# Performance work log

Measured on AMD Instinct MI355X. Metric: run time of the kernel, lower is better.

The kernel has to match this reference:

```python
import jax, jax.numpy as jnp
import numpy as np

B, DIM, IMG, HEADS, DH = 8, 512, 32, 8, 64
INNER = HEADS * DH  # == DIM, required by final reshape(b, n, c)
N = IMG * IMG
BN_EPS = 1e-5


def setup_inputs() -> dict:
    key = jax.random.key(0)
    ks = jax.random.split(key, 11)
    s = lambda k, sh: jax.random.normal(k, sh, jnp.float32) * 0.05
    return {
        "x": jax.random.normal(ks[0], (B, N, DIM), jnp.float32),
        # stacked q/k/v params, index 0=q, 1=k, 2=v
        "dw_w": s(ks[1], (3, DIM, 1, 3, 3)),   # depthwise conv kernels (OIHW, groups=DIM)
        "dw_b": s(ks[2], (3, DIM)),
        "bn_g": jnp.ones((3, DIM), jnp.float32) + s(ks[3], (3, DIM)),
        "bn_b": s(ks[4], (3, DIM)),
        "bn_m": s(ks[5], (3, DIM)),
        "bn_v": jnp.abs(jax.random.normal(ks[6], (3, DIM), jnp.float32)) + 1.0,
        "pw_w": s(ks[7], (3, INNER, DIM)),     # pointwise 1x1 conv weights
        "pw_b": s(ks[8], (3, INNER)),
        "out_w": s(ks[9], (DIM, INNER)),       # nn.Linear weight [out, in]
        "out_b": s(ks[10], (DIM,)),
    }


def _proj(x_img, dw_w, dw_b, bn_g, bn_b, bn_m, bn_v, pw_w, pw_b):
    # depthwise 3x3 conv, stride 1, pad 1
    y = jax.lax.conv_general_dilated(
        x_img, dw_w, (1, 1), [(1, 1), (1, 1)],
        dimension_numbers=("NCHW", "OIHW", "NCHW"), feature_group_count=DIM)
    y = y + dw_b[None, :, None, None]
    # eval-mode BatchNorm2d
    scale = bn_g / jnp.sqrt(bn_v + BN_EPS)
    y = (y - bn_m[None, :, None, None]) * scale[None, :, None, None] + bn_b[None, :, None, None]
    # pointwise 1x1 conv
    y = jnp.einsum("bchw,oc->bohw", y, pw_w) + pw_b[None, :, None, None]
    return y


def reference(x, dw_w, dw_b, bn_g, bn_b, bn_m, bn_v, pw_w, pw_b, out_w, out_b):
    b = x.shape[0]
    # b (l w) c -> b c l w
    xi = x.transpose(0, 2, 1).reshape(b, DIM, IMG, IMG)
    # q, k, v: b (h d) l w -> b h (l w) d
    qkv = [
        _proj(xi, dw_w[i], dw_b[i], bn_g[i], bn_b[i], bn_m[i], bn_v[i], pw_w[i], pw_b[i])
        .reshape(b, HEADS, DH, N).transpose(0, 1, 3, 2)
        for i in range(3)
    ]
    q, k, v = qkv
    att = jax.nn.softmax(jnp.einsum("bhnd,bhmd->bhnm", q, k) * (DH ** -0.5), axis=-1)
    out = jnp.einsum("bhnm,bhmd->bhnd", att, v)  # [b,h,n,d]
    out = out.transpose(0, 2, 1, 3).reshape(b, N, INNER)
    return out @ out_w.T + out_b  # to_out Linear (dropout=0)
```

## Files before the change

### kernel.cpp

```cpp
#include <hip/hip_runtime.h>
#include <hip/hip_bf16.h>

#define BB    8
#define DIMC  512
#define IMGS  32
#define NPIX  1024
#define NHEAD 8
#define DHEAD 64

typedef __attribute__((ext_vector_type(8))) short short8;
typedef __attribute__((ext_vector_type(4))) float float4v;

__device__ __forceinline__ float b2f(unsigned short u) {
  union { unsigned int i; float f; } c;
  c.i = ((unsigned int)u) << 16;
  return c.f;
}
__device__ __forceinline__ unsigned short f2b(float f) {
  union { float f; unsigned int u; } c;
  c.f = f;
  unsigned int r = c.u + 0x7fffu + ((c.u >> 16) & 1u);
  return (unsigned short)(r >> 16);
}

__device__ __forceinline__ void storeC(float* p, float v) { *p = v; }
__device__ __forceinline__ void storeC(unsigned short* p, float v) { *p = f2b(v); }

__device__ __forceinline__ void async16(const void* g, void* l) {
  __builtin_amdgcn_global_load_lds(
      (const __attribute__((address_space(1))) void*)g,
      (__attribute__((address_space(3))) void*)l, 16, 0, 0);
}

__global__ __launch_bounds__(256) void wcvt_kernel(
    const float* __restrict__ pw_w, const float* __restrict__ out_w,
    unsigned short* __restrict__ wbf) {
  const int i4 = (blockIdx.x * 256 + threadIdx.x) * 4;
  float4 v = (i4 < 3 * DIMC * DIMC)
                 ? *reinterpret_cast<const float4*>(pw_w + i4)
                 : *reinterpret_cast<const float4*>(out_w + (i4 - 3 * DIMC * DIMC));
  ushort4 o;
  o.x = f2b(v.x); o.y = f2b(v.y); o.z = f2b(v.z); o.w = f2b(v.w);
  *reinterpret_cast<ushort4*>(wbf + i4) = o;
}

__global__ __launch_bounds__(256) void dwbn_kernel(
    const float* __restrict__ x, const float* __restrict__ dw_w,
    const float* __restrict__ dw_b, const float* __restrict__ bn_g,
    const float* __restrict__ bn_b, const float* __restrict__ bn_m,
    const float* __restrict__ bn_v, unsigned short* __restrict__ z) {
  const int bx = blockIdx.x;
  const int b = bx >> 10, n = bx & (NPIX - 1);
  const int l = n >> 5, w = n & 31;
  const int c0 = threadIdx.x * 2;
  const float* xb = x + (size_t)b * NPIX * DIMC + c0;
  float2 xv[9];
  #pragma unroll
  for (int kh = 0; kh < 3; ++kh) {
    #pragma unroll
    for (int kw = 0; kw < 3; ++kw) {
      const int l2 = l + kh - 1, w2 = w + kw - 1;
      const bool ok = (l2 >= 0 && l2 < IMGS && w2 >= 0 && w2 < IMGS);
      xv[kh * 3 + kw] =
          ok ? *reinterpret_cast<const float2*>(xb + (size_t)(l2 * IMGS + w2) * DIMC)
             : make_float2(0.f, 0.f);
    }
  }
  #pragma unroll
  for (int i = 0; i < 3; ++i) {
    const int pc = i * DIMC + c0;
    const float* wp = dw_w + (size_t)pc * 9;
    float a0 = dw_b[pc], a1 = dw_b[pc + 1];
    #pragma unroll
    for (int k = 0; k < 9; ++k) {
      a0 = fmaf(wp[k], xv[k].x, a0);
      a1 = fmaf(wp[9 + k], xv[k].y, a1);
    }
    const float s0 = bn_g[pc] * rsqrtf(bn_v[pc] + 1e-5f);
    const float s1 = bn_g[pc + 1] * rsqrtf(bn_v[pc + 1] + 1e-5f);
    const float r0 = (a0 - bn_m[pc]) * s0 + bn_b[pc];
    const float r1 = (a1 - bn_m[pc + 1]) * s1 + bn_b[pc + 1];
    ushort2 st;
    st.x = f2b(r0);
    st.y = f2b(r1);
    *reinterpret_cast<ushort2*>(
        z + (((size_t)(i * BB + b)) * NPIX + n) * DIMC + c0) = st;
  }
}

template <typename CT>
__global__ __launch_bounds__(256) void gemm_mfma(
    const unsigned short* __restrict__ Abase,
    const unsigned short* __restrict__ Wbase,
    const float* __restrict__ biasBase, CT* __restrict__ Cbase) {
  __shared__ short As[8 * 64 * 8];
  __shared__ short Bs[8 * 64 * 8];
  const int bz = blockIdx.z;
  const int wi = bz >> 3;
  const short* A = (const short*)Abase + (size_t)bz * NPIX * DIMC;
  const short* W = (const short*)Wbase + (size_t)wi * DIMC * DIMC;
  const float* bias = biasBase + wi * DIMC;
  CT* C = Cbase + (size_t)bz * NPIX * DIMC;

  const int t = threadIdx.x;
  const int wv = t >> 6, lane = t & 63;
  const int lo = lane & 15, hi = lane >> 4;
  const int wm = wv >> 1, wn = wv & 1;
  const int m0 = blockIdx.y * 128, n0 = blockIdx.x * 128;

  float4v acc[4][4];
  #pragma unroll
  for (int i = 0; i < 4; ++i)
    #pragma unroll
    for (int j = 0; j < 4; ++j) acc[i][j] = {0.f, 0.f, 0.f, 0.f};

  for (int k0 = 0; k0 < DIMC; k0 += 32) {
    #pragma unroll
    for (int p = 0; p < 2; ++p) {
      const int sub = wv + p * 4;
      async16(A + (size_t)(m0 + sub * 16 + lo) * DIMC + k0 + hi * 8,
              As + (sub * 64 + lane) * 8);
      async16(W + (size_t)(n0 + sub * 16 + lo) * DIMC + k0 + hi * 8,
              Bs + (sub * 64 + lane) * 8);
    }
    __syncthreads();
    short8 af[4], bf[4];
    #pragma unroll
    for (int mt = 0; mt < 4; ++mt)
      af[mt] = *reinterpret_cast<const short8*>(As + ((wm * 4 + mt) * 64 + lane) * 8);
    #pragma unroll
    for (int nt = 0; nt < 4; ++nt)
      bf[nt] = *reinterpret_cast<const short8*>(Bs + ((wn * 4 + nt) * 64 + lane) * 8);
    #pragma unroll
    for (int mt = 0; mt < 4; ++mt)
      #pragma unroll
      for (int nt = 0; nt < 4; ++nt)
        acc[mt][nt] = __builtin_amdgcn_mfma_f32_16x16x32_bf16(af[mt], bf[nt],
                                                              acc[mt][nt], 0, 0, 0);
    __syncthreads();
  }

  float bv[4];
  #pragma unroll
  for (int nt = 0; nt < 4; ++nt) bv[nt] = bias[n0 + wn * 64 + nt * 16 + lo];
  #pragma unroll
  for (int mt = 0; mt < 4; ++mt) {
    #pragma unroll
    for (int r = 0; r < 4; ++r) {
      const int row = m0 + wm * 64 + mt * 16 + hi * 4 + r;
      CT* cp = C + (size_t)row * DIMC + n0 + wn * 64 + lo;
      #pragma unroll
      for (int nt = 0; nt < 4; ++nt) storeC(cp + nt * 16, acc[mt][nt][r] + bv[nt]);
    }
  }
}

__global__ __launch_bounds__(256) void vt_kernel(
    const unsigned short* __restrict__ v, unsigned short* __restrict__ vt) {
  __shared__ unsigned short tile[64][68];
  const int n0 = blockIdx.x * 64, h = blockIdx.y, b = blockIdx.z;
  const int t = threadIdx.x;
  const unsigned short* vb = v + (size_t)b * NPIX * DIMC + h * DHEAD;
  #pragma unroll
  for (int u = 0; u < 4; ++u) {
    const int lin = t + u * 256;
    const int row = lin >> 4, c4 = (lin & 15) * 4;
    *reinterpret_cast<ushort4*>(&tile[row][c4]) =
        *reinterpret_cast<const ushort4*>(vb + (size_t)(n0 + row) * DIMC + c4);
  }
  __syncthreads();
  unsigned short* vtb = vt + ((size_t)(b * NHEAD + h)) * DHEAD * NPIX;
  #pragma unroll
  for (int u = 0; u < 4; ++u) {
    const int lin = t + u * 256;
    const int d = lin >> 4, n4 = (lin & 15) * 4;
    ushort4 o;
    o.x = tile[n4 + 0][d];
    o.y = tile[n4 + 1][d];
    o.z = tile[n4 + 2][d];
    o.w = tile[n4 + 3][d];
    *reinterpret_cast<ushort4*>(vtb + (size_t)d * NPIX + n0 + n4) = o;
  }
}

__global__ __launch_bounds__(256) void attn_mfma(
    const unsigned short* __restrict__ qkv, const unsigned short* __restrict__ vt,
    unsigned short* __restrict__ attn_o) {
  __shared__ short Ks[8 * 64 * 8];
  __shared__ short VTs[8 * 64 * 8];
  __shared__ short Ps[4 * 16 * 72];

  const int qt = blockIdx.x, h = blockIdx.y, b = blockIdx.z;
  const int t = threadIdx.x;
  const int wv = t >> 6, lane = t & 63;
  const int lo = lane & 15, hi = lane >> 4;
  short* Ps_w = Ps + wv * 16 * 72;

  const short* qb = (const short*)qkv + ((size_t)(0 * BB + b) * NPIX) * DIMC + h * DHEAD;
  const short* kb = (const short*)qkv + ((size_t)(1 * BB + b) * NPIX) * DIMC + h * DHEAD;
  const short* vtb = (const short*)vt + ((size_t)(b * NHEAD + h)) * DHEAD * NPIX;

  short8 qfrag[2];
  #pragma unroll
  for (int cc = 0; cc < 2; ++cc)
    qfrag[cc] = *reinterpret_cast<const short8*>(
        qb + (size_t)(qt * 64 + wv * 16 + lo) * DIMC + cc * 32 + hi * 8);

  float m_prev[4], l_run[4];
  float4v oacc[4];
  #pragma unroll
  for (int r = 0; r < 4; ++r) { m_prev[r] = -3.0e38f; l_run[r] = 0.f; }
  #pragma unroll
  for (int dt = 0; dt < 4; ++dt) oacc[dt] = {0.f, 0.f, 0.f, 0.f};

  for (int kt = 0; kt < 16; ++kt) {
    #pragma unroll
    for (int p = 0; p < 2; ++p) {
      const int sub = wv + p * 4;
      const int nk = sub >> 1, cc = sub & 1;
      async16(kb + (size_t)(kt * 64 + nk * 16 + lo) * DIMC + cc * 32 + hi * 8,
              Ks + (sub * 64 + lane) * 8);
      async16(vtb + (size_t)(nk * 16 + lo) * NPIX + kt * 64 + cc * 32 + hi * 8,
              VTs + (sub * 64 + lane) * 8);
    }
    __syncthreads();

    float4v sacc[4];
    #pragma unroll
    for (int nt = 0; nt < 4; ++nt) {
      sacc[nt] = {0.f, 0.f, 0.f, 0.f};
      const short8 k0 = *reinterpret_cast<const short8*>(Ks + ((nt * 2 + 0) * 64 + lane) * 8);
      const short8 k1 = *reinterpret_cast<const short8*>(Ks + ((nt * 2 + 1) * 64 + lane) * 8);
      sacc[nt] = __builtin_amdgcn_mfma_f32_16x16x32_bf16(qfrag[0], k0, sacc[nt], 0, 0, 0);
      sacc[nt] = __builtin_amdgcn_mfma_f32_16x16x32_bf16(qfrag[1], k1, sacc[nt], 0, 0, 0);
    }

    float alpha[4];
    #pragma unroll
    for (int r = 0; r < 4; ++r) {
      const float s0 = sacc[0][r] * 0.125f, s1 = sacc[1][r] * 0.125f;
      const float s2 = sacc[2][r] * 0.125f, s3 = sacc[3][r] * 0.125f;
      float ml = fmaxf(fmaxf(s0, s1), fmaxf(s2, s3));
      ml = fmaxf(ml, __shfl_xor(ml, 1));
      ml = fmaxf(ml, __shfl_xor(ml, 2));
      ml = fmaxf(ml, __shfl_xor(ml, 4));
      ml = fmaxf(ml, __shfl_xor(ml, 8));
      const float mn = fmaxf(m_prev[r], ml);
      const float al = __expf(m_prev[r] - mn);
      const float p0 = __expf(s0 - mn), p1 = __expf(s1 - mn);
      const float p2 = __expf(s2 - mn), p3 = __expf(s3 - mn);
      short* pr = Ps_w + (hi * 4 + r) * 72 + lo;
      pr[0]  = (short)f2b(p0);
      pr[16] = (short)f2b(p1);
      pr[32] = (short)f2b(p2);
      pr[48] = (short)f2b(p3);
      float ps = p0 + p1 + p2 + p3;
      ps += __shfl_xor(ps, 1);
      ps += __shfl_xor(ps, 2);
      ps += __shfl_xor(ps, 4);
      ps += __shfl_xor(ps, 8);
      l_run[r] = l_run[r] * al + ps;
      m_prev[r] = mn;
      alpha[r] = al;
    }
    #pragma unroll
    for (int dt = 0; dt < 4; ++dt)
      #pragma unroll
      for (int r = 0; r < 4; ++r) oacc[dt][r] *= alpha[r];
    __syncthreads();

    const short8 pf0 = *reinterpret_cast<const short8*>(Ps_w + lo * 72 + 0 + hi * 8);
    const short8 pf1 = *reinterpret_cast<const short8*>(Ps_w + lo * 72 + 32 + hi * 8);
    #pragma unroll
    for (int dt = 0; dt < 4; ++dt) {
      const short8 v0 = *reinterpret_cast<const short8*>(VTs + ((dt * 2 + 0) * 64 + lane) * 8);
      const short8 v1 = *reinterpret_cast<const short8*>(VTs + ((dt * 2 + 1) * 64 + lane) * 8);
      oacc[dt] = __builtin_amdgcn_mfma_f32_16x16x32_bf16(pf0, v0, oacc[dt], 0, 0, 0);
      oacc[dt] = __builtin_amdgcn_mfma_f32_16x16x32_bf16(pf1, v1, oacc[dt], 0, 0, 0);
    }
    __syncthreads();
  }

  float inv[4];
  #pragma unroll
  for (int r = 0; r < 4; ++r) inv[r] = 1.0f / l_run[r];
  #pragma unroll
  for (int dt = 0; dt < 4; ++dt) {
    #pragma unroll
    for (int r = 0; r < 4; ++r) {
      const int row = qt * 64 + wv * 16 + hi * 4 + r;
      attn_o[((size_t)b * NPIX + row) * DIMC + h * DHEAD + dt * 16 + lo] =
          f2b(oacc[dt][r] * inv[r]);
    }
  }
}

extern "C" void kernel_launch(void* const* d_in, const int* in_sizes, int n_in,
                              void* d_out, int out_size, void* d_ws, size_t ws_size,
                              hipStream_t stream) {
  const float* x    = (const float*)d_in[0];
  const float* dw_w = (const float*)d_in[1];
  const float* dw_b = (const float*)d_in[2];
  const float* bn_g = (const float*)d_in[3];
  const float* bn_b = (const float*)d_in[4];
  const float* bn_m = (const float*)d_in[5];
  const float* bn_v = (const float*)d_in[6];
  const float* pw_w = (const float*)d_in[7];
  const float* pw_b = (const float*)d_in[8];
  const float* out_w = (const float*)d_in[9];
  const float* out_b = (const float*)d_in[10];
  float* out = (float*)d_out;

  unsigned short* z    = (unsigned short*)d_ws;
  unsigned short* qkv  = z + (size_t)3 * BB * NPIX * DIMC;
  unsigned short* wbf  = qkv + (size_t)3 * BB * NPIX * DIMC;
  unsigned short* vtb  = z;
  unsigned short* attn_o = z + (size_t)BB * NHEAD * DHEAD * NPIX;

  wcvt_kernel<<<dim3(1024), 256, 0, stream>>>(pw_w, out_w, wbf);
  dwbn_kernel<<<dim3(BB * NPIX), 256, 0, stream>>>(x, dw_w, dw_b, bn_g, bn_b,
                                                   bn_m, bn_v, z);
  gemm_mfma<unsigned short><<<dim3(4, 8, 24), 256, 0, stream>>>(z, wbf, pw_b, qkv);
  vt_kernel<<<dim3(16, NHEAD, BB), 256, 0, stream>>>(
      qkv + (size_t)2 * BB * NPIX * DIMC, vtb);
  attn_mfma<<<dim3(16, NHEAD, BB), 256, 0, stream>>>(qkv, vtb, attn_o);
  gemm_mfma<float><<<dim3(4, 8, 8), 256, 0, stream>>>(
      attn_o, wbf + (size_t)3 * DIMC * DIMC, out_b, out);
}
```

Measured before the change: 245.1 us.

## Split attention keys across waves, drop online max, fold softmax scale into Q

The attention kernel is restructured so each wave owns a quarter of the keys for all 64 query rows, with private LDS staging. This removes the block-wide barriers inside the key loop, and the partial outputs and row sums are reduced through LDS at the end. The running max and rescaling of online softmax are removed and raw exp(s) is used, with the 1/sqrt(d) scale folded into the Q projection weights and bias during weight conversion. This cuts exp, shuffle and rescale work, but exp can overflow if scores ever grow large, and the epilogue now needs an LDS reduction across waves.

```diff
diff --git a/kernel.cpp b/kernel.cpp
--- a/kernel.cpp
+++ b/kernel.cpp
@@ -32,16 +32,28 @@
       (__attribute__((address_space(3))) void*)l, 16, 0, 0);
 }
 
+#define WAITCNT_VM0   0x0F70
+#define WAITCNT_LGKM0 0xC07F
+
 __global__ __launch_bounds__(256) void wcvt_kernel(
     const float* __restrict__ pw_w, const float* __restrict__ out_w,
-    unsigned short* __restrict__ wbf) {
+    const float* __restrict__ pw_b, unsigned short* __restrict__ wbf,
+    float* __restrict__ bb) {
   const int i4 = (blockIdx.x * 256 + threadIdx.x) * 4;
   float4 v = (i4 < 3 * DIMC * DIMC)
                  ? *reinterpret_cast<const float4*>(pw_w + i4)
                  : *reinterpret_cast<const float4*>(out_w + (i4 - 3 * DIMC * DIMC));
+  const float sc = (i4 < DIMC * DIMC) ? 0.125f : 1.0f;
   ushort4 o;
-  o.x = f2b(v.x); o.y = f2b(v.y); o.z = f2b(v.z); o.w = f2b(v.w);
+  o.x = f2b(v.x * sc); o.y = f2b(v.y * sc); o.z = f2b(v.z * sc); o.w = f2b(v.w * sc);
   *reinterpret_cast<ushort4*>(wbf + i4) = o;
+  if (blockIdx.x == 0) {
+    #pragma unroll
+    for (int k = 0; k < 6; ++k) {
+      const int idx = threadIdx.x + k * 256;
+      bb[idx] = pw_b[idx] * (idx < DIMC ? 0.125f : 1.0f);
+    }
+  }
 }
 
 __global__ __launch_bounds__(256) void dwbn_kernel(
@@ -183,114 +195,145 @@
   }
 }
 
-__global__ __launch_bounds__(256) void attn_mfma(
+__global__ __launch_bounds__(256, 2) void attn_mfma(
     const unsigned short* __restrict__ qkv, const unsigned short* __restrict__ vt,
     unsigned short* __restrict__ attn_o) {
-  __shared__ short Ks[8 * 64 * 8];
-  __shared__ short VTs[8 * 64 * 8];
-  __shared__ short Ps[4 * 16 * 72];
-
+  __shared__ char sm[53248];
   const int qt = blockIdx.x, h = blockIdx.y, b = blockIdx.z;
   const int t = threadIdx.x;
   const int wv = t >> 6, lane = t & 63;
   const int lo = lane & 15, hi = lane >> 4;
-  short* Ps_w = Ps + wv * 16 * 72;
+
+  char* wbase = sm + wv * 13312;
+  short* Ks = (short*)(wbase);
+  short* VTs = (short*)(wbase + 4096);
+  short* Ps = (short*)(wbase + 8192);
 
   const short* qb = (const short*)qkv + ((size_t)(0 * BB + b) * NPIX) * DIMC + h * DHEAD;
   const short* kb = (const short*)qkv + ((size_t)(1 * BB + b) * NPIX) * DIMC + h * DHEAD;
   const short* vtb = (const short*)vt + ((size_t)(b * NHEAD + h)) * DHEAD * NPIX;
 
-  short8 qfrag[2];
-  #pragma unroll
-  for (int cc = 0; cc < 2; ++cc)
-    qfrag[cc] = *reinterpret_cast<const short8*>(
-        qb + (size_t)(qt * 64 + wv * 16 + lo) * DIMC + cc * 32 + hi * 8);
-
-  float m_prev[4], l_run[4];
-  float4v oacc[4];
-  #pragma unroll
-  for (int r = 0; r < 4; ++r) { m_prev[r] = -3.0e38f; l_run[r] = 0.f; }
-  #pragma unroll
-  for (int dt = 0; dt < 4; ++dt) oacc[dt] = {0.f, 0.f, 0.f, 0.f};
-
-  for (int kt = 0; kt < 16; ++kt) {
-    #pragma unroll
-    for (int p = 0; p < 2; ++p) {
-      const int sub = wv + p * 4;
-      const int nk = sub >> 1, cc = sub & 1;
-      async16(kb + (size_t)(kt * 64 + nk * 16 + lo) * DIMC + cc * 32 + hi * 8,
-              Ks + (sub * 64 + lane) * 8);
-      async16(vtb + (size_t)(nk * 16 + lo) * NPIX + kt * 64 + cc * 32 + hi * 8,
-              VTs + (sub * 64 + lane) * 8);
-    }
+  short8 qf[4][2];
+  #pragma unroll
+  for (int mt = 0; mt < 4; ++mt)
+    #pragma unroll
+    for (int cc = 0; cc < 2; ++cc)
+      qf[mt][cc] = *reinterpret_cast<const short8*>(
+          qb + (size_t)(qt * 64 + mt * 16 + lo) * DIMC + cc * 32 + hi * 8);
+
+  float4v oacc[4][4];
+  float4v lsum[4];
+  #pragma unroll
+  for (int mt = 0; mt < 4; ++mt) {
+    lsum[mt] = {0.f, 0.f, 0.f, 0.f};
+    #pragma unroll
+    for (int dt = 0; dt < 4; ++dt) oacc[mt][dt] = {0.f, 0.f, 0.f, 0.f};
+  }
+
+  const int n0 = wv * 256;
+  for (int kt = 0; kt < 8; ++kt) {
+    const int kbase = n0 + kt * 32;
+    __builtin_amdgcn_s_waitcnt(WAITCNT_LGKM0);
+    __builtin_amdgcn_sched_barrier(0);
+    #pragma unroll
+    for (int s = 0; s < 4; ++s) {
+      const int nt = s >> 1, cc = s & 1;
+      async16(kb + (size_t)(kbase + nt * 16 + lo) * DIMC + cc * 32 + hi * 8,
+              Ks + (s * 64 + lane) * 8);
+    }
+    #pragma unroll
+    for (int dt = 0; dt < 4; ++dt)
+      async16(vtb + (size_t)(dt * 16 + lo) * NPIX + kbase + hi * 8,
+              VTs + (dt * 64 + lane) * 8);
+    __builtin_amdgcn_sched_barrier(0);
+    __builtin_amdgcn_s_waitcnt(WAITCNT_VM0);
+    __builtin_amdgcn_sched_barrier(0);
+
+    short8 kf[2][2];
+    #pragma unroll
+    for (int nt = 0; nt < 2; ++nt)
+      #pragma unroll
+      for (int cc = 0; cc < 2; ++cc)
+        kf[nt][cc] = *reinterpret_cast<const short8*>(Ks + ((nt * 2 + cc) * 64 + lane) * 8);
+    float4v sacc[4][2];
+    #pragma unroll
+    for (int mt = 0; mt < 4; ++mt)
+      #pragma unroll
+      for (int nt = 0; nt < 2; ++nt) {
+        sacc[mt][nt] = {0.f, 0.f, 0.f, 0.f};
+        sacc[mt][nt] = __builtin_amdgcn_mfma_f32_16x16x32_bf16(qf[mt][0], kf[nt][0],
+                                                               sacc[mt][nt], 0, 0, 0);
+        sacc[mt][nt] = __builtin_amdgcn_mfma_f32_16x16x32_bf16(qf[mt][1], kf[nt][1],
+                                                               sacc[mt][nt], 0, 0, 0);
+      }
+
+    #pragma unroll
+    for (int mt = 0; mt < 4; ++mt)
+      #pragma unroll
+      for (int nt = 0; nt < 2; ++nt)
+        #pragma unroll
+        for (int r = 0; r < 4; ++r) {
+          const float p = __expf(sacc[mt][nt][r]);
+          Ps[(mt * 16 + hi * 4 + r) * 40 + nt * 16 + lo] = (short)f2b(p);
+          lsum[mt][r] += p;
+        }
+
+    short8 vf[4];
+    #pragma unroll
+    for (int dt = 0; dt < 4; ++dt)
+      vf[dt] = *reinterpret_cast<const short8*>(VTs + (dt * 64 + lane) * 8);
+    #pragma unroll
+    for (int mt = 0; mt < 4; ++mt) {
+      const short8 pf = *reinterpret_cast<const short8*>(Ps + (mt * 16 + lo) * 40 + hi * 8);
+      #pragma unroll
+      for (int dt = 0; dt < 4; ++dt)
+        oacc[mt][dt] = __builtin_amdgcn_mfma_f32_16x16x32_bf16(pf, vf[dt],
+                                                               oacc[mt][dt], 0, 0, 0);
+    }
+  }
+
+  #pragma unroll
+  for (int mt = 0; mt < 4; ++mt)
+    #pragma unroll
+    for (int r = 0; r < 4; ++r) {
+      float v = lsum[mt][r];
+      v += __shfl_xor(v, 1);
+      v += __shfl_xor(v, 2);
+      v += __shfl_xor(v, 4);
+      v += __shfl_xor(v, 8);
+      lsum[mt][r] = v;
+    }
+
+  float* Obuf = (float*)sm;
+  float* lbuf = (float*)(sm + 16384);
+  float* linv = (float*)(sm + 17408);
+  __syncthreads();
+  if (lo == 0) {
+    #pragma unroll
+    for (int mt = 0; mt < 4; ++mt)
+      #pragma unroll
+      for (int r = 0; r < 4; ++r) lbuf[wv * 64 + mt * 16 + hi * 4 + r] = lsum[mt][r];
+  }
+  __syncthreads();
+  if (t < 64) linv[t] = 1.0f / (lbuf[t] + lbuf[64 + t] + lbuf[128 + t] + lbuf[192 + t]);
+
+  unsigned short* aob = attn_o + ((size_t)b * NPIX + qt * 64) * DIMC + h * DHEAD;
+  #pragma unroll
+  for (int mt = 0; mt < 4; ++mt) {
     __syncthreads();
-
-    float4v sacc[4];
-    #pragma unroll
-    for (int nt = 0; nt < 4; ++nt) {
-      sacc[nt] = {0.f, 0.f, 0.f, 0.f};
-      const short8 k0 = *reinterpret_cast<const short8*>(Ks + ((nt * 2 + 0) * 64 + lane) * 8);
-      const short8 k1 = *reinterpret_cast<const short8*>(Ks + ((nt * 2 + 1) * 64 + lane) * 8);
-      sacc[nt] = __builtin_amdgcn_mfma_f32_16x16x32_bf16(qfrag[0], k0, sacc[nt], 0, 0, 0);
-      sacc[nt] = __builtin_amdgcn_mfma_f32_16x16x32_bf16(qfrag[1], k1, sacc[nt], 0, 0, 0);
-    }
-
-    float alpha[4];
-    #pragma unroll
-    for (int r = 0; r < 4; ++r) {
-      const float s0 = sacc[0][r] * 0.125f, s1 = sacc[1][r] * 0.125f;
-      const float s2 = sacc[2][r] * 0.125f, s3 = sacc[3][r] * 0.125f;
-      float ml = fmaxf(fmaxf(s0, s1), fmaxf(s2, s3));
-      ml = fmaxf(ml, __shfl_xor(ml, 1));
-      ml = fmaxf(ml, __shfl_xor(ml, 2));
-      ml = fmaxf(ml, __shfl_xor(ml, 4));
-      ml = fmaxf(ml, __shfl_xor(ml, 8));
-      const float mn = fmaxf(m_prev[r], ml);
-      const float al = __expf(m_prev[r] - mn);
-      const float p0 = __expf(s0 - mn), p1 = __expf(s1 - mn);
-      const float p2 = __expf(s2 - mn), p3 = __expf(s3 - mn);
-      short* pr = Ps_w + (hi * 4 + r) * 72 + lo;
-      pr[0]  = (short)f2b(p0);
-      pr[16] = (short)f2b(p1);
-      pr[32] = (short)f2b(p2);
-      pr[48] = (short)f2b(p3);
-      float ps = p0 + p1 + p2 + p3;
-      ps += __shfl_xor(ps, 1);
-      ps += __shfl_xor(ps, 2);
-      ps += __shfl_xor(ps, 4);
-      ps += __shfl_xor(ps, 8);
-      l_run[r] = l_run[r] * al + ps;
-      m_prev[r] = mn;
-      alpha[r] = al;
-    }
     #pragma unroll
     for (int dt = 0; dt < 4; ++dt)
       #pragma unroll
-      for (int r = 0; r < 4; ++r) oacc[dt][r] *= alpha[r];
+      for (int r = 0; r < 4; ++r)
+        Obuf[wv * 1024 + (dt * 4 + r) * 64 + lane] = oacc[mt][dt][r];
     __syncthreads();
-
-    const short8 pf0 = *reinterpret_cast<const short8*>(Ps_w + lo * 72 + 0 + hi * 8);
-    const short8 pf1 = *reinterpret_cast<const short8*>(Ps_w + lo * 72 + 32 + hi * 8);
-    #pragma unroll
-    for (int dt = 0; dt < 4; ++dt) {
-      const short8 v0 = *reinterpret_cast<const short8*>(VTs + ((dt * 2 + 0) * 64 + lane) * 8);
-      const short8 v1 = *reinterpret_cast<const short8*>(VTs + ((dt * 2 + 1) * 64 + lane) * 8);
-      oacc[dt] = __builtin_amdgcn_mfma_f32_16x16x32_bf16(pf0, v0, oacc[dt], 0, 0, 0);
-      oacc[dt] = __builtin_amdgcn_mfma_f32_16x16x32_bf16(pf1, v1, oacc[dt], 0, 0, 0);
-    }
-    __syncthreads();
-  }
-
-  float inv[4];
-  #pragma unroll
-  for (int r = 0; r < 4; ++r) inv[r] = 1.0f / l_run[r];
-  #pragma unroll
-  for (int dt = 0; dt < 4; ++dt) {
-    #pragma unroll
-    for (int r = 0; r < 4; ++r) {
-      const int row = qt * 64 + wv * 16 + hi * 4 + r;
-      attn_o[((size_t)b * NPIX + row) * DIMC + h * DHEAD + dt * 16 + lo] =
-          f2b(oacc[dt][r] * inv[r]);
+    #pragma unroll
+    for (int k2 = 0; k2 < 4; ++k2) {
+      const int e = t + k2 * 256;
+      const float sum2 = Obuf[e] + Obuf[1024 + e] + Obuf[2048 + e] + Obuf[3072 + e];
+      const int dt = e >> 8, r = (e >> 6) & 3, le = e & 63;
+      const int row = mt * 16 + (le >> 4) * 4 + r, d = dt * 16 + (le & 15);
+      aob[(size_t)row * DIMC + d] = f2b(sum2 * linv[row]);
     }
   }
 }
@@ -311,16 +354,17 @@
   const float* out_b = (const float*)d_in[10];
   float* out = (float*)d_out;
 
-  unsigned short* z    = (unsigned short*)d_ws;
-  unsigned short* qkv  = z + (size_t)3 * BB * NPIX * DIMC;
-  unsigned short* wbf  = qkv + (size_t)3 * BB * NPIX * DIMC;
-  unsigned short* vtb  = z;
+  unsigned short* z   = (unsigned short*)d_ws;
+  unsigned short* qkv = z + (size_t)3 * BB * NPIX * DIMC;
+  unsigned short* wbf = qkv + (size_t)3 * BB * NPIX * DIMC;
+  float* bb = (float*)(wbf + (size_t)4 * DIMC * DIMC);
+  unsigned short* vtb = z;
   unsigned short* attn_o = z + (size_t)BB * NHEAD * DHEAD * NPIX;
 
-  wcvt_kernel<<<dim3(1024), 256, 0, stream>>>(pw_w, out_w, wbf);
+  wcvt_kernel<<<dim3(1024), 256, 0, stream>>>(pw_w, out_w, pw_b, wbf, bb);
   dwbn_kernel<<<dim3(BB * NPIX), 256, 0, stream>>>(x, dw_w, dw_b, bn_g, bn_b,
                                                    bn_m, bn_v, z);
-  gemm_mfma<unsigned short><<<dim3(4, 8, 24), 256, 0, stream>>>(z, wbf, pw_b, qkv);
+  gemm_mfma<unsigned short><<<dim3(4, 8, 24), 256, 0, stream>>>(z, wbf, bb, qkv);
   vt_kernel<<<dim3(16, NHEAD, BB), 256, 0, stream>>>(
       qkv + (size_t)2 * BB * NPIX * DIMC, vtb);
   attn_mfma<<<dim3(16, NHEAD, BB), 256, 0, stream>>>(qkv, vtb, attn_o);
```

New measurement: 230.1 us. 6.1% less time.
